# Performance work log

Hardware: AMD Instinct MI355X
Metric: run time of the kernel (lower is better)

## Reference

```python
import jax, jax.numpy as jnp
import numpy as np

BATCH = 16384
MAX_ACTIVE = 32
FEAT = 768
HIDDEN = 1024


def setup_inputs() -> dict:
    key = jax.random.key(0)
    k1, k2, k3, k4, k5, k6 = jax.random.split(key, 6)
    stm = jax.random.randint(k1, (BATCH, MAX_ACTIVE), 0, FEAT, dtype=jnp.int32)
    nstm = jax.random.randint(k2, (BATCH, MAX_ACTIVE), 0, FEAT, dtype=jnp.int32)
    # Linear params (PyTorch layout: weight is (out_features, in_features))
    ft_w = jax.random.normal(k3, (HIDDEN, FEAT), dtype=jnp.float32) * 0.05
    ft_b = jax.random.normal(k4, (HIDDEN,), dtype=jnp.float32) * 0.05
    out_w = jax.random.normal(k5, (1, 2 * HIDDEN), dtype=jnp.float32) * 0.05
    out_b = jax.random.normal(k6, (1,), dtype=jnp.float32) * 0.05
    return {"stm": stm, "nstm": nstm, "ft_w": ft_w, "ft_b": ft_b,
            "out_w": out_w, "out_b": out_b}


def sparse_to_dense(indices: jnp.ndarray, size: int = FEAT) -> jnp.ndarray:
    """(B, max_active) int indices with -1 padding -> (B, size) 0/1 float32."""
    b = indices.shape[0]
    valid = (indices >= 0).astype(jnp.float32)          # (B, A)
    cols = jnp.clip(indices, 0, size - 1)               # padded -> col 0, masked by `valid`
    rows = jnp.arange(b, dtype=jnp.int32)[:, None]      # (B, 1) broadcast
    dense = jnp.zeros((b, size), dtype=jnp.float32)
    # .max matches torch's set-to-1 semantics even if duplicate indices occur
    return dense.at[rows, cols].max(valid)


def reference(stm, nstm, ft_w, ft_b, out_w, out_b):
    stm_d = sparse_to_dense(stm)                        # (B, 768)
    nstm_d = sparse_to_dense(nstm)                      # (B, 768)
    stm_h = stm_d @ ft_w.T + ft_b                       # (B, H)
    nstm_h = nstm_d @ ft_w.T + ft_b                     # (B, H)
    hidden = jnp.concatenate([stm_h, nstm_h], axis=1)   # (B, 2H)
    hidden = jnp.clip(hidden, 0.0, 1.0)
    return jax.nn.sigmoid(hidden @ out_w.T + out_b)     # (B, 1)
```

## Files before the change

kernel.cpp:

```cpp
#include <hip/hip_runtime.h>
#include <hip/hip_bf16.h>
#include <stdint.h>

#define BATCH 16384
#define MAXA 32
#define FEAT 768
#define HIDDEN 1024

__global__ __launch_bounds__(256) void scale_k(const float* __restrict__ ftw,
                                               float* __restrict__ scale,
                                               float* __restrict__ invsc,
                                               uint8_t* __restrict__ wQ) {
  if (blockIdx.x == HIDDEN) {
    if (threadIdx.x < 64) {
      uint4 v; v.x = v.y = v.z = v.w = 0x80808080u;
      ((uint4*)(wQ + (size_t)FEAT * HIDDEN))[threadIdx.x] = v;
    }
    return;
  }
  const int h = blockIdx.x;
  float a = 0.f;
#pragma unroll
  for (int p = 0; p < 3; ++p)
    a = fmaxf(a, fabsf(ftw[h * FEAT + p * 256 + threadIdx.x]));
#pragma unroll
  for (int off = 32; off > 0; off >>= 1)
    a = fmaxf(a, __shfl_xor(a, off, 64));
  __shared__ float red[4];
  if ((threadIdx.x & 63) == 0) red[threadIdx.x >> 6] = a;
  __syncthreads();
  if (threadIdx.x == 0) {
    float m = fmaxf(fmaxf(red[0], red[1]), fmaxf(red[2], red[3]));
    m = fmaxf(m, 1e-20f);
    scale[h] = m / 127.f;
    invsc[h] = 127.f / m;
  }
}

__global__ __launch_bounds__(256) void tilequant(const float* __restrict__ ftw,
                                                 const float* __restrict__ invsc,
                                                 uint8_t* __restrict__ wQ) {
  const int f0 = (blockIdx.x % (FEAT / 64)) * 64;
  const int h0 = (blockIdx.x / (FEAT / 64)) * 64;
  __shared__ uint8_t tile[64][80];
  __shared__ float inv[64];
  if (threadIdx.x < 64) inv[threadIdx.x] = invsc[h0 + threadIdx.x];
  __syncthreads();
  const int ff = threadIdx.x & 63;
  const int hb = threadIdx.x >> 6;
#pragma unroll
  for (int p = 0; p < 16; ++p) {
    int hh = p * 4 + hb;
    float w = ftw[(size_t)(h0 + hh) * FEAT + f0 + ff];
    int q = __float2int_rn(w * inv[hh]);
    tile[ff][hh] = (uint8_t)(q + 128);
  }
  __syncthreads();
  const int fs = threadIdx.x >> 2, part = threadIdx.x & 3;
  uint4 v = *(const uint4*)&tile[fs][part * 16];
  *(uint4*)(wQ + (size_t)(f0 + fs) * HIDDEN + h0 + part * 16) = v;
}

__device__ __forceinline__ void acc16(uint32_t* acc, uint4 w) {
  acc[0] += __builtin_amdgcn_perm(0u, w.x, 0x0c010c00u);
  acc[1] += __builtin_amdgcn_perm(0u, w.x, 0x0c030c02u);
  acc[2] += __builtin_amdgcn_perm(0u, w.y, 0x0c010c00u);
  acc[3] += __builtin_amdgcn_perm(0u, w.y, 0x0c030c02u);
  acc[4] += __builtin_amdgcn_perm(0u, w.z, 0x0c010c00u);
  acc[5] += __builtin_amdgcn_perm(0u, w.z, 0x0c030c02u);
  acc[6] += __builtin_amdgcn_perm(0u, w.w, 0x0c010c00u);
  acc[7] += __builtin_amdgcn_perm(0u, w.w, 0x0c030c02u);
}

__global__ __launch_bounds__(256) void nn_fwd(
    const int* __restrict__ stm, const int* __restrict__ nstm,
    const uint8_t* __restrict__ wQ, const float* __restrict__ scale,
    const float* __restrict__ bias, const float* __restrict__ outw,
    const float* __restrict__ outb, float* __restrict__ out)
{
  const int lane = threadIdx.x & 63;
  const int row  = blockIdx.x * 4 + (threadIdx.x >> 6);
  const int half = lane >> 5;
  const int pos  = lane & 31;

  const int* __restrict__ src = half ? nstm : stm;
  int idx = src[row * MAXA + pos];
  bool valid = idx >= 0;
#pragma unroll
  for (int j = 0; j < 31; ++j) {
    int other = __shfl(idx, (half << 5) | j, 64);
    if (j < pos && other == idx) valid = false;
  }
  const int fmap = valid ? idx : FEAT;

  uint32_t accs[8], accn[8];
#pragma unroll
  for (int k = 0; k < 8; ++k) { accs[k] = 0u; accn[k] = 0u; }

#pragma unroll
  for (int j = 0; j < 32; ++j) {
    int fs_ = __builtin_amdgcn_readlane(fmap, j);
    int fn_ = __builtin_amdgcn_readlane(fmap, 32 + j);
    const uint4* ps = (const uint4*)(wQ + (size_t)fs_ * HIDDEN);
    const uint4* pn = (const uint4*)(wQ + (size_t)fn_ * HIDDEN);
    uint4 ws_ = ps[lane];
    uint4 wn_ = pn[lane];
    acc16(accs, ws_);
    acc16(accn, wn_);
  }

  const int DB = 32 * 128;

  const int hbase = lane * 16;
  float sc[16], bb[16], ows[16], own[16];
  {
    const float4* s4 = (const float4*)(scale + hbase);
    const float4* b4 = (const float4*)(bias + hbase);
    const float4* oS = (const float4*)(outw + hbase);
    const float4* oN = (const float4*)(outw + HIDDEN + hbase);
#pragma unroll
    for (int q = 0; q < 4; ++q) {
      float4 v;
      v = s4[q]; sc[4*q]=v.x; sc[4*q+1]=v.y; sc[4*q+2]=v.z; sc[4*q+3]=v.w;
      v = b4[q]; bb[4*q]=v.x; bb[4*q+1]=v.y; bb[4*q+2]=v.z; bb[4*q+3]=v.w;
      v = oS[q]; ows[4*q]=v.x; ows[4*q+1]=v.y; ows[4*q+2]=v.z; ows[4*q+3]=v.w;
      v = oN[q]; own[4*q]=v.x; own[4*q+1]=v.y; own[4*q+2]=v.z; own[4*q+3]=v.w;
    }
  }
  float partial = 0.f;
#pragma unroll
  for (int k = 0; k < 16; ++k) {
    uint32_t as = accs[k >> 1], an = accn[k >> 1];
    int qs = (int)((k & 1) ? (as >> 16) : (as & 0xffffu)) - DB;
    int qn = (int)((k & 1) ? (an >> 16) : (an & 0xffffu)) - DB;
    float hs = fminf(fmaxf(fmaf((float)qs, sc[k], bb[k]), 0.f), 1.f);
    float hn = fminf(fmaxf(fmaf((float)qn, sc[k], bb[k]), 0.f), 1.f);
    partial += hs * ows[k] + hn * own[k];
  }
#pragma unroll
  for (int off = 32; off > 0; off >>= 1)
    partial += __shfl_down(partial, off, 64);
  if (lane == 0) {
    float y = partial + outb[0];
    out[row] = 1.f / (1.f + __expf(-y));
  }
}

extern "C" void kernel_launch(void* const* d_in, const int* in_sizes, int n_in,
                              void* d_out, int out_size, void* d_ws, size_t ws_size,
                              hipStream_t stream) {
  const int*   stm  = (const int*)d_in[0];
  const int*   nstm = (const int*)d_in[1];
  const float* ftw  = (const float*)d_in[2];
  const float* ftb  = (const float*)d_in[3];
  const float* outw = (const float*)d_in[4];
  const float* outb = (const float*)d_in[5];

  uint8_t* wQ    = (uint8_t*)d_ws;
  float*   scale = (float*)(wQ + (size_t)(FEAT + 1) * HIDDEN);
  float*   invsc = scale + HIDDEN;

  scale_k<<<HIDDEN + 1, 256, 0, stream>>>(ftw, scale, invsc, wQ);
  tilequant<<<(FEAT / 64) * (HIDDEN / 64), 256, 0, stream>>>(ftw, invsc, wQ);
  nn_fwd<<<BATCH / 4, 256, 0, stream>>>(stm, nstm, wQ, scale, ftb, outw, outb,
                                        (float*)d_out);
}
```

Measured before the change: 120.1 us.

## Sort feature indices per half-wave, batch gathers, and cap registers for occupancy

```diff
diff --git a/kernel.cpp b/kernel.cpp
--- a/kernel.cpp
+++ b/kernel.cpp
@@ -72,7 +72,7 @@
   acc[7] += __builtin_amdgcn_perm(0u, w.w, 0x0c030c02u);
 }
 
-__global__ __launch_bounds__(256) void nn_fwd(
+__global__ __launch_bounds__(256, 6) void nn_fwd(
     const int* __restrict__ stm, const int* __restrict__ nstm,
     const uint8_t* __restrict__ wQ, const float* __restrict__ scale,
     const float* __restrict__ bias, const float* __restrict__ outw,
@@ -91,51 +91,61 @@
     int other = __shfl(idx, (half << 5) | j, 64);
     if (j < pos && other == idx) valid = false;
   }
-  const int fmap = valid ? idx : FEAT;
+  int fmap = valid ? idx : FEAT;
+
+#pragma unroll
+  for (int k = 2; k <= 32; k <<= 1) {
+#pragma unroll
+    for (int j = k >> 1; j > 0; j >>= 1) {
+      int other = __shfl_xor(fmap, j, 64);
+      bool lower = (pos & j) == 0;
+      bool desc  = (pos & k) != 0;
+      int mn = min(fmap, other), mx = max(fmap, other);
+      fmap = (lower != desc) ? mn : mx;
+    }
+  }
 
   uint32_t accs[8], accn[8];
 #pragma unroll
   for (int k = 0; k < 8; ++k) { accs[k] = 0u; accn[k] = 0u; }
 
 #pragma unroll
-  for (int j = 0; j < 32; ++j) {
-    int fs_ = __builtin_amdgcn_readlane(fmap, j);
-    int fn_ = __builtin_amdgcn_readlane(fmap, 32 + j);
-    const uint4* ps = (const uint4*)(wQ + (size_t)fs_ * HIDDEN);
-    const uint4* pn = (const uint4*)(wQ + (size_t)fn_ * HIDDEN);
-    uint4 ws_ = ps[lane];
-    uint4 wn_ = pn[lane];
-    acc16(accs, ws_);
-    acc16(accn, wn_);
+  for (int jb = 0; jb < 32; jb += 4) {
+    uint4 ws[4], wn[4];
+#pragma unroll
+    for (int u = 0; u < 4; ++u) {
+      int fs_ = __builtin_amdgcn_readlane(fmap, jb + u);
+      int fn_ = __builtin_amdgcn_readlane(fmap, 32 + jb + u);
+      ws[u] = ((const uint4*)(wQ + (size_t)fs_ * HIDDEN))[lane];
+      wn[u] = ((const uint4*)(wQ + (size_t)fn_ * HIDDEN))[lane];
+    }
+#pragma unroll
+    for (int u = 0; u < 4; ++u) { acc16(accs, ws[u]); acc16(accn, wn[u]); }
   }
 
   const int DB = 32 * 128;
 
   const int hbase = lane * 16;
-  float sc[16], bb[16], ows[16], own[16];
-  {
-    const float4* s4 = (const float4*)(scale + hbase);
-    const float4* b4 = (const float4*)(bias + hbase);
-    const float4* oS = (const float4*)(outw + hbase);
-    const float4* oN = (const float4*)(outw + HIDDEN + hbase);
-#pragma unroll
-    for (int q = 0; q < 4; ++q) {
-      float4 v;
-      v = s4[q]; sc[4*q]=v.x; sc[4*q+1]=v.y; sc[4*q+2]=v.z; sc[4*q+3]=v.w;
-      v = b4[q]; bb[4*q]=v.x; bb[4*q+1]=v.y; bb[4*q+2]=v.z; bb[4*q+3]=v.w;
-      v = oS[q]; ows[4*q]=v.x; ows[4*q+1]=v.y; ows[4*q+2]=v.z; ows[4*q+3]=v.w;
-      v = oN[q]; own[4*q]=v.x; own[4*q+1]=v.y; own[4*q+2]=v.z; own[4*q+3]=v.w;
-    }
-  }
+  const float4* s4 = (const float4*)(scale + hbase);
+  const float4* b4 = (const float4*)(bias + hbase);
+  const float4* oS = (const float4*)(outw + hbase);
+  const float4* oN = (const float4*)(outw + HIDDEN + hbase);
   float partial = 0.f;
 #pragma unroll
-  for (int k = 0; k < 16; ++k) {
-    uint32_t as = accs[k >> 1], an = accn[k >> 1];
-    int qs = (int)((k & 1) ? (as >> 16) : (as & 0xffffu)) - DB;
-    int qn = (int)((k & 1) ? (an >> 16) : (an & 0xffffu)) - DB;
-    float hs = fminf(fmaxf(fmaf((float)qs, sc[k], bb[k]), 0.f), 1.f);
-    float hn = fminf(fmaxf(fmaf((float)qn, sc[k], bb[k]), 0.f), 1.f);
-    partial += hs * ows[k] + hn * own[k];
+  for (int q = 0; q < 4; ++q) {
+    float4 sv = s4[q], bv = b4[q], ov = oS[q], nv = oN[q];
+    const float* sp = &sv.x; const float* bp = &bv.x;
+    const float* op = &ov.x; const float* np = &nv.x;
+#pragma unroll
+    for (int e = 0; e < 4; ++e) {
+      int k = q * 4 + e;
+      uint32_t as = accs[k >> 1], an = accn[k >> 1];
+      int qs = (int)((k & 1) ? (as >> 16) : (as & 0xffffu)) - DB;
+      int qn = (int)((k & 1) ? (an >> 16) : (an & 0xffffu)) - DB;
+      float hs = fminf(fmaxf(fmaf((float)qs, sp[e], bp[e]), 0.f), 1.f);
+      float hn = fminf(fmaxf(fmaf((float)qn, sp[e], bp[e]), 0.f), 1.f);
+      partial += hs * op[e] + hn * np[e];
+    }
   }
 #pragma unroll
   for (int off = 32; off > 0; off >>= 1)
```

Measured after the change: 120.3 us. About the same (+0.2%).
